# Optimization experiments

Hardware: AMD Instinct MI355X
Metric: run time of the kernel (lower is better)

## Reference

```python
import jax, jax.numpy as jnp
import numpy as np

T, B, N = 2048, 32, 1024   # time, batch, dan_hidden_size
H = 8                      # multihead_size
N2 = 128                   # attention_hidden_size
K = N // H                 # N_H = 128 per-head dim
K2 = N2 // H               # N2_H = 16 per-head attention dim


def setup_inputs() -> dict:
    key = jax.random.key(0)
    ks = jax.random.split(key, 10)
    s_n = 1.0 / np.sqrt(N)
    s_k = 1.0 / np.sqrt(K)
    s_k2 = 1.0 / np.sqrt(K2)
    return {
        "hyp": jax.random.normal(ks[0], (T, B, N), dtype=jnp.float32),
        # H independent per-head linears N -> K, stacked: (H, K, N)
        "Wmh": jax.random.uniform(ks[1], (H, K, N), minval=-s_n, maxval=s_n, dtype=jnp.float32),
        "bmh": jax.random.uniform(ks[2], (H, K), minval=-s_n, maxval=s_n, dtype=jnp.float32),
        # shared W: K -> K2
        "W": jax.random.uniform(ks[3], (K2, K), minval=-s_k, maxval=s_k, dtype=jnp.float32),
        "bW": jax.random.uniform(ks[4], (K2,), minval=-s_k, maxval=s_k, dtype=jnp.float32),
        # shared W_m: K -> K2
        "Wm": jax.random.uniform(ks[5], (K2, K), minval=-s_k, maxval=s_k, dtype=jnp.float32),
        "bWm": jax.random.uniform(ks[6], (K2,), minval=-s_k, maxval=s_k, dtype=jnp.float32),
        # shared W_h: K2 -> 1
        "Wh": jax.random.uniform(ks[7], (K2,), minval=-s_k2, maxval=s_k2, dtype=jnp.float32),
        "bWh": jax.random.uniform(ks[8], (), minval=-s_k2, maxval=s_k2, dtype=jnp.float32),
        "dan_hidden_size": N,
        "attention_hidden_size": N2,
        "multihead_size": H,
    }


def reference(hyp, Wmh, bmh, W, bW, Wm, bWm, Wh, bWh,
              dan_hidden_size, attention_hidden_size, multihead_size):
    # Per-head projections, all heads at once: (B, T, H, K)
    X = jnp.einsum('tbn,hkn->bthk', hyp, Wmh) + bmh
    # mean over time (original x.mean(0)): (B, H, K)
    m = X.mean(axis=1)
    # tanh-gated additive scoring: (B, T, H, K2)
    g = jnp.tanh(jnp.einsum('bthk,qk->bthq', X, W) + bW) \
        * jnp.tanh(jnp.einsum('bhk,qk->bhq', m, Wm) + bWm)[:, None]
    # scalar score per (b, t, h), softmax over time
    s = jnp.einsum('bthq,q->bth', g, Wh) + bWh
    a = jax.nn.softmax(s, axis=1)                       # (B, T, H)
    # attention-weighted sum over time: (B, H, K)
    c = jnp.einsum('bth,bthk->bhk', a, X)
    # concat heads along feature dim (head-major order, matches torch.cat)
    Bsz = c.shape[0]
    return c.reshape(Bsz, -1)                            # (B, N)
```

## Files before the change

### kernel.cpp

```cpp
#include <hip/hip_runtime.h>
#include <hip/hip_bf16.h>

#define T_DIM 2048
#define B_DIM 32
#define N_DIM 1024
#define H_DIM 8
#define K_DIM 128
#define Q_DIM 16

typedef __bf16 bf16x8 __attribute__((ext_vector_type(8)));
typedef __bf16 bf16x4 __attribute__((ext_vector_type(4)));
typedef float  f32x4  __attribute__((ext_vector_type(4)));

__device__ inline bf16x8 cvt8(float4 a, float4 b) {
    bf16x8 r;
    r[0] = (__bf16)a.x; r[1] = (__bf16)a.y; r[2] = (__bf16)a.z; r[3] = (__bf16)a.w;
    r[4] = (__bf16)b.x; r[5] = (__bf16)b.y; r[6] = (__bf16)b.z; r[7] = (__bf16)b.w;
    return r;
}

__global__ __launch_bounds__(256)
void cvt_f32_bf16(const float* __restrict__ s, __bf16* __restrict__ d)
{
    const long i = ((long)blockIdx.x * 256 + threadIdx.x) * 8;
    float4 a = *(const float4*)(s + i);
    float4 b = *(const float4*)(s + i + 4);
    *(bf16x8*)(d + i) = cvt8(a, b);
}

__global__ __launch_bounds__(512, 1)
void gemm_x_8ph(const __bf16* __restrict__ A, const __bf16* __restrict__ Bw,
                const float* __restrict__ bias, __bf16* __restrict__ X,
                float* __restrict__ mpart)
{
    __shared__ __bf16 ldsA[2][16384];
    __shared__ __bf16 ldsB[2][16384];
    __bf16* ldsAf = &ldsA[0][0];
    __bf16* ldsBf = &ldsB[0][0];

    const int tid  = threadIdx.x;
    const int lane = tid & 63;
    const int w    = tid >> 6;
    const int wm   = w >> 2;
    const int wn   = w & 3;

    const int bid  = blockIdx.x;
    const int wgid = (bid & 7) * 128 + (bid >> 3);
    const int bm   = wgid >> 2;
    const int bn   = wgid & 3;
    const long row0 = (long)bm * 256;
    const long col0 = (long)bn * 256;

    const int srow = w * 8 + (lane >> 3);
    const int scol = ((lane & 7) ^ (lane >> 3)) * 8;
    const __bf16* Ag = A  + (row0 + srow) * 1024 + scol;
    const __bf16* Bg = Bw + (col0 + srow) * 1024 + scol;
    const int ldst = w * 512;

    const int fr = lane & 15;
    const int g2 = lane >> 4;
    const int x7 = lane & 7;

    const __bf16* aK0 = ldsAf + (wm * 128 + fr) * 64 + ((g2    ) ^ x7) * 8;
    const __bf16* aK1 = ldsAf + (wm * 128 + fr) * 64 + ((4 + g2) ^ x7) * 8;
    const __bf16* bK0 = ldsBf + (wn * 64  + fr) * 64 + ((g2    ) ^ x7) * 8;
    const __bf16* bK1 = ldsBf + (wn * 64  + fr) * 64 + ((4 + g2) ^ x7) * 8;

    f32x4 acc[8][4];
    #pragma unroll
    for (int i = 0; i < 8; ++i)
        #pragma unroll
        for (int j = 0; j < 4; ++j)
            acc[i][j] = f32x4{0.f, 0.f, 0.f, 0.f};

    #define GLDA(SRC_, DST_) __builtin_amdgcn_global_load_lds( \
        (const __attribute__((address_space(1))) void*)(SRC_), \
        (__attribute__((address_space(3))) void*)(DST_), 16, 0, 0)

    #pragma unroll
    for (int j = 0; j < 2; ++j) GLDA(Ag + (long)j * 65536,          ldsAf + j * 4096 + ldst);
    #pragma unroll
    for (int j = 0; j < 2; ++j) GLDA(Ag + 131072 + (long)j * 65536, ldsAf + 8192 + j * 4096 + ldst);
    #pragma unroll
    for (int j = 0; j < 2; ++j) GLDA(Bg + (long)j * 65536,          ldsBf + j * 4096 + ldst);
    #pragma unroll
    for (int j = 0; j < 2; ++j) GLDA(Bg + 131072 + (long)j * 65536, ldsBf + 8192 + j * 4096 + ldst);
    #pragma unroll
    for (int j = 0; j < 2; ++j) GLDA(Bg + 64 + (long)j * 65536,          ldsBf + 16384 + j * 4096 + ldst);
    #pragma unroll
    for (int j = 0; j < 2; ++j) GLDA(Bg + 64 + 131072 + (long)j * 65536, ldsBf + 16384 + 8192 + j * 4096 + ldst);
    asm volatile("s_waitcnt vmcnt(4)" ::: "memory");
    __builtin_amdgcn_sched_barrier(0);
    __builtin_amdgcn_s_barrier();

    const __bf16* AgN = Ag + 64;
    const __bf16* BgN = Bg + 128;

    #define MFMA16(AF_, BF_, OFF_)                                             \
        __builtin_amdgcn_s_setprio(1);                                         \
        _Pragma("unroll") for (int mi = 0; mi < 4; ++mi)                       \
            _Pragma("unroll") for (int ni = 0; ni < 4; ++ni)                   \
                acc[mi + (OFF_)][ni] = __builtin_amdgcn_mfma_f32_16x16x32_bf16(\
                    BF_[ni], AF_[mi], acc[mi + (OFF_)][ni], 0, 0, 0);          \
        __builtin_amdgcn_s_setprio(0);

    #define LGKM0()                                                            \
        asm volatile("s_waitcnt lgkmcnt(0)" ::: "memory");                     \
        __builtin_amdgcn_sched_barrier(0);

    #define KTBODY(SO_, SN_, KO_, STGA_, STGB_, VM_)                           \
    {                                                                          \
        bf16x8 a0[4], b0[4], a0h[4], b1[4], a1[4], a1h[4];                     \
        _Pragma("unroll") for (int mi = 0; mi < 4; ++mi)                       \
            a0[mi] = *(const bf16x8*)(aK0 + (SO_) + mi * 1024);                \
        _Pragma("unroll") for (int ni = 0; ni < 4; ++ni)                       \
            b0[ni] = *(const bf16x8*)(bK0 + (SO_) + ni * 1024);                \
        if (STGA_) {                                                           \
            _Pragma("unroll") for (int j = 0; j < 2; ++j)                      \
                GLDA(AgN + (KO_) + (long)j * 65536,                            \
                     ldsAf + (SN_) + j * 4096 + ldst);                         \
        }                                                                      \
        __builtin_amdgcn_s_barrier();                                          \
        LGKM0();                                                               \
        MFMA16(a0, b0, 0);                                                     \
        __builtin_amdgcn_s_barrier();                                          \
        _Pragma("unroll") for (int mi = 0; mi < 4; ++mi)                       \
            a0h[mi] = *(const bf16x8*)(aK1 + (SO_) + mi * 1024);               \
        _Pragma("unroll") for (int ni = 0; ni < 4; ++ni)                       \
            b1[ni]  = *(const bf16x8*)(bK1 + (SO_) + ni * 1024);               \
        if (STGA_) {                                                           \
            _Pragma("unroll") for (int j = 0; j < 2; ++j)                      \
                GLDA(AgN + (KO_) + 131072 + (long)j * 65536,                   \
                     ldsAf + (SN_) + 8192 + j * 4096 + ldst);                  \
        }                                                                      \
        __builtin_amdgcn_s_barrier();                                          \
        LGKM0();                                                               \
        MFMA16(a0h, b1, 0);                                                    \
        __builtin_amdgcn_s_barrier();                                          \
        _Pragma("unroll") for (int mi = 0; mi < 4; ++mi)                       \
            a1[mi] = *(const bf16x8*)(aK0 + (SO_) + (mi + 4) * 1024);          \
        if (STGB_) {                                                           \
            _Pragma("unroll") for (int j = 0; j < 2; ++j)                      \
                GLDA(BgN + (KO_) + (long)j * 65536,                            \
                     ldsBf + (SO_) + j * 4096 + ldst);                         \
        }                                                                      \
        __builtin_amdgcn_s_barrier();                                          \
        LGKM0();                                                               \
        MFMA16(a1, b0, 4);                                                     \
        __builtin_amdgcn_s_barrier();                                          \
        _Pragma("unroll") for (int mi = 0; mi < 4; ++mi)                       \
            a1h[mi] = *(const bf16x8*)(aK1 + (SO_) + (mi + 4) * 1024);         \
        if (STGB_) {                                                           \
            _Pragma("unroll") for (int j = 0; j < 2; ++j)                      \
                GLDA(BgN + (KO_) + 131072 + (long)j * 65536,                   \
                     ldsBf + (SO_) + 8192 + j * 4096 + ldst);                  \
        }                                                                      \
        if ((VM_) == 4)      { asm volatile("s_waitcnt vmcnt(4)" ::: "memory"); } \
        else if ((VM_) == 0) { asm volatile("s_waitcnt vmcnt(0)" ::: "memory"); } \
        __builtin_amdgcn_sched_barrier(0);                                     \
        __builtin_amdgcn_s_barrier();                                          \
        LGKM0();                                                               \
        MFMA16(a1h, b1, 4);                                                    \
        __builtin_amdgcn_s_barrier();                                          \
    }

    #pragma unroll 1
    for (int ii = 0; ii < 7; ++ii) {
        KTBODY(0,     16384, 0,  1, 1, 4);
        KTBODY(16384, 0,     64, 1, 1, 4);
        AgN += 128; BgN += 128;
    }
    KTBODY(0,     16384, 0, 1, 0, 0);
    KTBODY(16384, 0,     0, 0, 0, -1);
    #undef KTBODY
    #undef MFMA16
    #undef LGKM0
    #undef GLDA

    const int g4 = lane >> 4;
    const long colb = col0 + wn * 64 + g4 * 4;

    float4 bias4[4];
    #pragma unroll
    for (int ni = 0; ni < 4; ++ni)
        bias4[ni] = *(const float4*)(bias + colb + ni * 16);

    f32x4 msum[2][4];
    #pragma unroll
    for (int bh = 0; bh < 2; ++bh)
        #pragma unroll
        for (int ni = 0; ni < 4; ++ni)
            msum[bh][ni] = f32x4{0.f, 0.f, 0.f, 0.f};

    #pragma unroll
    for (int mi = 0; mi < 8; ++mi) {
        const long row = row0 + wm * 128 + mi * 16 + fr;
        #pragma unroll
        for (int ni = 0; ni < 4; ++ni) {
            f32x4 xv;
            xv[0] = acc[mi][ni][0] + bias4[ni].x;
            xv[1] = acc[mi][ni][1] + bias4[ni].y;
            xv[2] = acc[mi][ni][2] + bias4[ni].z;
            xv[3] = acc[mi][ni][3] + bias4[ni].w;
            bf16x4 xb;
            xb[0] = (__bf16)xv[0]; xb[1] = (__bf16)xv[1];
            xb[2] = (__bf16)xv[2]; xb[3] = (__bf16)xv[3];
            *(bf16x4*)(X + row * 1024 + colb + ni * 16) = xb;
            msum[mi & 1][ni] += xv;
        }
    }

    float* ldsf = (float*)ldsAf;
    __syncthreads();
    if (wm == 1) {
        #pragma unroll
        for (int bh = 0; bh < 2; ++bh)
            #pragma unroll
            for (int ni = 0; ni < 4; ++ni)
                *(f32x4*)(ldsf + (bh * 16 + fr) * 256 + wn * 64 + ni * 16 + g4 * 4) = msum[bh][ni];
    }
    __syncthreads();
    if (wm == 0) {
        #pragma unroll
        for (int bh = 0; bh < 2; ++bh) {
            const int b = bh * 16 + fr;
            #pragma unroll
            for (int ni = 0; ni < 4; ++ni) {
                f32x4 other = *(const f32x4*)(ldsf + b * 256 + wn * 64 + ni * 16 + g4 * 4);
                f32x4 tot = msum[bh][ni] + other;
                *(f32x4*)(mpart + ((long)bm * 32 + b) * 1024 + colb + ni * 16) = tot;
            }
        }
    }
}

__global__ __launch_bounds__(256)
void gate2_k(const float* __restrict__ mpart, const float* __restrict__ Wm,
             const float* __restrict__ bWm, float* __restrict__ g2)
{
    __shared__ float mrow[1024];
    const int b = blockIdx.x;
    const int j4 = threadIdx.x * 4;
    f32x4 s = f32x4{0.f, 0.f, 0.f, 0.f};
    for (int bm = 0; bm < 256; ++bm)
        s += *(const f32x4*)(mpart + ((long)bm * 32 + b) * 1024 + j4);
    mrow[j4 + 0] = s[0] * (1.0f / 2048.0f);
    mrow[j4 + 1] = s[1] * (1.0f / 2048.0f);
    mrow[j4 + 2] = s[2] * (1.0f / 2048.0f);
    mrow[j4 + 3] = s[3] * (1.0f / 2048.0f);
    __syncthreads();
    if (threadIdx.x < 128) {
        const int h = threadIdx.x >> 4;
        const int q = threadIdx.x & 15;
        float d = bWm[q];
        #pragma unroll 8
        for (int k = 0; k < 128; ++k) d += mrow[h * 128 + k] * Wm[q * 128 + k];
        g2[(b * 8 + h) * 16 + q] = tanhf(d);
    }
}

__global__ __launch_bounds__(256)
void attn_part(const __bf16* __restrict__ X, const float* __restrict__ W,
               const float* __restrict__ bW, const float* __restrict__ g2,
               const float* __restrict__ Wh,
               float* __restrict__ partC, float* __restrict__ partML)
{
    __shared__ float sch[64];
    __shared__ float pl[64];
    __shared__ float red[1024];
    __shared__ float scal[3];

    const int tid  = threadIdx.x;
    const int lane = tid & 63;
    const int w    = tid >> 6;
    const int bx   = blockIdx.x;
    const int bh   = bx & 255;
    const int tc   = bx >> 8;
    const int b    = bh >> 3;
    const int h    = bh & 7;
    const int q    = lane & 15;
    const int g4   = lane >> 4;

    if (tid == 0) { scal[0] = -1e30f; scal[1] = 0.f; scal[2] = 0.f; }

    bf16x8 bfr[4];
    #pragma unroll
    for (int c = 0; c < 4; ++c) {
        const float* wp = W + q * 128 + c * 32 + g4 * 8;
        float4 w0 = *(const float4*)wp;
        float4 w1 = *(const float4*)(wp + 4);
        bfr[c] = cvt8(w0, w1);
    }
    const float whq = Wh[q];
    const float bWv = bW[q];
    const float gq  = g2[(b * 8 + h) * 16 + q];

    const long t0 = (long)tc * 256;
    const __bf16* xp = X + ((t0 + w * 16 + q) * 32 + b) * 1024 + h * 128 + g4 * 8;
    const int tr = tid >> 5;
    const int kq = tid & 31;
    const __bf16* xa = X + ((t0 + tr) * 32 + b) * 1024 + h * 128 + kq * 4;

    float c0 = 0.f, c1 = 0.f, c2 = 0.f, c3 = 0.f;

    __syncthreads();

    #pragma unroll 1
    for (int ch = 0; ch < 4; ++ch) {
        bf16x8 afr[4];
        #pragma unroll
        for (int c = 0; c < 4; ++c) afr[c] = *(const bf16x8*)(xp + c * 32);
        f32x4 acc = f32x4{0.f, 0.f, 0.f, 0.f};
        #pragma unroll
        for (int c = 0; c < 4; ++c)
            acc = __builtin_amdgcn_mfma_f32_16x16x32_bf16(afr[c], bfr[c], acc, 0, 0, 0);
        #pragma unroll
        for (int r = 0; r < 4; ++r) {
            float val = tanhf(acc[r] + bWv) * gq * whq;
            val += __shfl_xor(val, 1);
            val += __shfl_xor(val, 2);
            val += __shfl_xor(val, 4);
            val += __shfl_xor(val, 8);
            if (q == 0) sch[w * 16 + g4 * 4 + r] = val;
        }
        __syncthreads();

        if (tid < 64) {
            float v = sch[tid];
            float mx = v;
            #pragma unroll
            for (int off = 1; off < 64; off <<= 1)
                mx = fmaxf(mx, __shfl_xor(mx, off));
            const float mold = scal[0];
            const float newm = fmaxf(mold, mx);
            const float f    = __expf(mold - newm);
            const float p    = __expf(v - newm);
            pl[tid] = p;
            float ps = p;
            #pragma unroll
            for (int off = 1; off < 64; off <<= 1)
                ps += __shfl_xor(ps, off);
            if (tid == 0) {
                scal[0] = newm;
                scal[1] = f;
                scal[2] = scal[2] * f + ps;
            }
        }
        __syncthreads();

        const float f = scal[1];
        if (f != 1.0f) { c0 *= f; c1 *= f; c2 *= f; c3 *= f; }
        #pragma unroll
        for (int i = 0; i < 8; ++i) {
            const float p = pl[tr + 8 * i];
            bf16x4 xv = *(const bf16x4*)(xa + (long)(8 * i) * 32768);
            c0 += p * (float)xv[0];
            c1 += p * (float)xv[1];
            c2 += p * (float)xv[2];
            c3 += p * (float)xv[3];
        }
        __syncthreads();

        xp += 64 * 32768;
        xa += 64 * 32768;
    }

    red[tr * 128 + kq * 4 + 0] = c0;
    red[tr * 128 + kq * 4 + 1] = c1;
    red[tr * 128 + kq * 4 + 2] = c2;
    red[tr * 128 + kq * 4 + 3] = c3;
    __syncthreads();
    if (tid < 128) {
        float s = 0.f;
        #pragma unroll
        for (int r = 0; r < 8; ++r) s += red[r * 128 + tid];
        partC[((long)bh * 8 + tc) * 128 + tid] = s;
    }
    if (tid == 0) {
        partML[(bh * 8 + tc) * 2 + 0] = scal[0];
        partML[(bh * 8 + tc) * 2 + 1] = scal[2];
    }
}

__global__ __launch_bounds__(128)
void attn_merge(const float* __restrict__ partC, const float* __restrict__ partML,
                float* __restrict__ out)
{
    __shared__ float wgt[8];
    __shared__ float lsum;
    const int bh = blockIdx.x;
    const int k  = threadIdx.x;
    if (k == 0) {
        float m = -1e30f;
        #pragma unroll
        for (int tc = 0; tc < 8; ++tc) m = fmaxf(m, partML[(bh * 8 + tc) * 2]);
        float l = 0.f;
        #pragma unroll
        for (int tc = 0; tc < 8; ++tc) {
            float e = __expf(partML[(bh * 8 + tc) * 2] - m);
            wgt[tc] = e;
            l += partML[(bh * 8 + tc) * 2 + 1] * e;
        }
        lsum = l;
    }
    __syncthreads();
    float s = 0.f;
    #pragma unroll
    for (int tc = 0; tc < 8; ++tc)
        s += partC[((long)bh * 8 + tc) * 128 + k] * wgt[tc];
    const int b = bh >> 3;
    const int h = bh & 7;
    out[b * 1024 + h * 128 + k] = s / lsum;
}

extern "C" void kernel_launch(void* const* d_in, const int* in_sizes, int n_in,
                              void* d_out, int out_size, void* d_ws, size_t ws_size,
                              hipStream_t stream)
{
    const float* hyp = (const float*)d_in[0];
    const float* Wmh = (const float*)d_in[1];
    const float* bmh = (const float*)d_in[2];
    const float* W   = (const float*)d_in[3];
    const float* bW  = (const float*)d_in[4];
    const float* Wm  = (const float*)d_in[5];
    const float* bWm = (const float*)d_in[6];
    const float* Wh  = (const float*)d_in[7];
    float* out = (float*)d_out;

    char* ws = (char*)d_ws;
    const size_t SZ_X   = 134217728;
    const size_t SZ_AB  = 134217728;
    const size_t SZ_BB  = 2097152;
    const size_t SZ_MP  = 33554432;
    const size_t SZ_G2  = 16384;
    const size_t SZ_PC  = 1048576;
    const size_t SZ_PM  = 16384;

    size_t off = 0;
    __bf16* X      = (__bf16*)(ws + off); off += SZ_X;
    __bf16* Ab     = (__bf16*)(ws + off); off += SZ_AB;
    __bf16* Bb     = (__bf16*)(ws + off); off += SZ_BB;
    float*  mpart  = (float*) (ws + off); off += SZ_MP;
    float*  g2     = (float*) (ws + off); off += SZ_G2;
    float*  partC  = (float*) (ws + off); off += SZ_PC;
    float*  partML = (float*) (ws + off); off += SZ_PM;

    cvt_f32_bf16<<<32768, 256, 0, stream>>>(hyp, Ab);
    cvt_f32_bf16<<<512,   256, 0, stream>>>(Wmh, Bb);
    gemm_x_8ph<<<1024, 512, 0, stream>>>(Ab, Bb, bmh, X, mpart);
    gate2_k<<<32, 256, 0, stream>>>(mpart, Wm, bWm, g2);
    attn_part<<<2048, 256, 0, stream>>>(X, W, bW, g2, Wh, partC, partML);
    attn_merge<<<256, 128, 0, stream>>>(partC, partML, out);
}
```

Baseline: 298.8 us.

## Shrink GEMM tile to 128x256 with K=32 stages for multi-block occupancy

```diff
diff --git a/kernel.cpp b/kernel.cpp
--- a/kernel.cpp
+++ b/kernel.cpp
@@ -28,15 +28,14 @@
     *(bf16x8*)(d + i) = cvt8(a, b);
 }
 
-__global__ __launch_bounds__(512, 1)
+__global__ __launch_bounds__(512, 4)
 void gemm_x_8ph(const __bf16* __restrict__ A, const __bf16* __restrict__ Bw,
                 const float* __restrict__ bias, __bf16* __restrict__ X,
                 float* __restrict__ mpart)
 {
-    __shared__ __bf16 ldsA[2][16384];
-    __shared__ __bf16 ldsB[2][16384];
-    __bf16* ldsAf = &ldsA[0][0];
-    __bf16* ldsBf = &ldsB[0][0];
+    __shared__ char ldsraw[49152];
+    __bf16* ldsAf = (__bf16*)ldsraw;
+    __bf16* ldsBf = (__bf16*)(ldsraw + 16384);
 
     const int tid  = threadIdx.x;
     const int lane = tid & 63;
@@ -45,30 +44,26 @@
     const int wn   = w & 3;
 
     const int bid  = blockIdx.x;
-    const int wgid = (bid & 7) * 128 + (bid >> 3);
+    const int wgid = (bid & 7) * 256 + (bid >> 3);
     const int bm   = wgid >> 2;
     const int bn   = wgid & 3;
-    const long row0 = (long)bm * 256;
+    const long row0 = (long)bm * 128;
     const long col0 = (long)bn * 256;
 
-    const int srow = w * 8 + (lane >> 3);
-    const int scol = ((lane & 7) ^ (lane >> 3)) * 8;
+    const int srow = w * 16 + (lane >> 2);
+    const int scol = ((lane & 3) ^ ((lane >> 2) & 3)) * 8;
     const __bf16* Ag = A  + (row0 + srow) * 1024 + scol;
     const __bf16* Bg = Bw + (col0 + srow) * 1024 + scol;
     const int ldst = w * 512;
 
     const int fr = lane & 15;
     const int g2 = lane >> 4;
-    const int x7 = lane & 7;
-
-    const __bf16* aK0 = ldsAf + (wm * 128 + fr) * 64 + ((g2    ) ^ x7) * 8;
-    const __bf16* aK1 = ldsAf + (wm * 128 + fr) * 64 + ((4 + g2) ^ x7) * 8;
-    const __bf16* bK0 = ldsBf + (wn * 64  + fr) * 64 + ((g2    ) ^ x7) * 8;
-    const __bf16* bK1 = ldsBf + (wn * 64  + fr) * 64 + ((4 + g2) ^ x7) * 8;
-
-    f32x4 acc[8][4];
-    #pragma unroll
-    for (int i = 0; i < 8; ++i)
+    const __bf16* aK0 = ldsAf + (wm * 64 + fr) * 32 + ((g2 ^ (fr & 3)) * 8);
+    const __bf16* bK0 = ldsBf + (wn * 64 + fr) * 32 + ((g2 ^ (fr & 3)) * 8);
+
+    f32x4 acc[4][4];
+    #pragma unroll
+    for (int i = 0; i < 4; ++i)
         #pragma unroll
         for (int j = 0; j < 4; ++j)
             acc[i][j] = f32x4{0.f, 0.f, 0.f, 0.f};
@@ -77,103 +72,59 @@
         (const __attribute__((address_space(1))) void*)(SRC_), \
         (__attribute__((address_space(3))) void*)(DST_), 16, 0, 0)
 
-    #pragma unroll
-    for (int j = 0; j < 2; ++j) GLDA(Ag + (long)j * 65536,          ldsAf + j * 4096 + ldst);
-    #pragma unroll
-    for (int j = 0; j < 2; ++j) GLDA(Ag + 131072 + (long)j * 65536, ldsAf + 8192 + j * 4096 + ldst);
-    #pragma unroll
-    for (int j = 0; j < 2; ++j) GLDA(Bg + (long)j * 65536,          ldsBf + j * 4096 + ldst);
-    #pragma unroll
-    for (int j = 0; j < 2; ++j) GLDA(Bg + 131072 + (long)j * 65536, ldsBf + 8192 + j * 4096 + ldst);
-    #pragma unroll
-    for (int j = 0; j < 2; ++j) GLDA(Bg + 64 + (long)j * 65536,          ldsBf + 16384 + j * 4096 + ldst);
-    #pragma unroll
-    for (int j = 0; j < 2; ++j) GLDA(Bg + 64 + 131072 + (long)j * 65536, ldsBf + 16384 + 8192 + j * 4096 + ldst);
-    asm volatile("s_waitcnt vmcnt(4)" ::: "memory");
+    GLDA(Ag, ldsAf + ldst);
+    #pragma unroll
+    for (int j = 0; j < 2; ++j) GLDA(Bg + (long)j * 131072, ldsBf + j * 4096 + ldst);
+    GLDA(Ag + 32, ldsAf + 4096 + ldst);
+    #pragma unroll
+    for (int j = 0; j < 2; ++j) GLDA(Bg + 32 + (long)j * 131072, ldsBf + 8192 + j * 4096 + ldst);
+    asm volatile("s_waitcnt vmcnt(3)" ::: "memory");
     __builtin_amdgcn_sched_barrier(0);
     __builtin_amdgcn_s_barrier();
 
     const __bf16* AgN = Ag + 64;
-    const __bf16* BgN = Bg + 128;
-
-    #define MFMA16(AF_, BF_, OFF_)                                             \
+    const __bf16* BgN = Bg + 64;
+
+    #define LGKM0()                                                            \
+        asm volatile("s_waitcnt lgkmcnt(0)" ::: "memory");                     \
+        __builtin_amdgcn_sched_barrier(0);
+
+    #define KTBODY(SOA_, SOB_, KO_, STG_, VM_)                                 \
+    {                                                                          \
+        bf16x8 a0[4], b0[4];                                                   \
+        _Pragma("unroll") for (int mi = 0; mi < 4; ++mi)                       \
+            a0[mi] = *(const bf16x8*)(aK0 + (SOA_) + mi * 512);                \
+        _Pragma("unroll") for (int ni = 0; ni < 4; ++ni)                       \
+            b0[ni] = *(const bf16x8*)(bK0 + (SOB_) + ni * 512);                \
+        __builtin_amdgcn_s_barrier();                                          \
+        LGKM0();                                                               \
         __builtin_amdgcn_s_setprio(1);                                         \
         _Pragma("unroll") for (int mi = 0; mi < 4; ++mi)                       \
             _Pragma("unroll") for (int ni = 0; ni < 4; ++ni)                   \
-                acc[mi + (OFF_)][ni] = __builtin_amdgcn_mfma_f32_16x16x32_bf16(\
-                    BF_[ni], AF_[mi], acc[mi + (OFF_)][ni], 0, 0, 0);          \
-        __builtin_amdgcn_s_setprio(0);
-
-    #define LGKM0()                                                            \
-        asm volatile("s_waitcnt lgkmcnt(0)" ::: "memory");                     \
-        __builtin_amdgcn_sched_barrier(0);
-
-    #define KTBODY(SO_, SN_, KO_, STGA_, STGB_, VM_)                           \
-    {                                                                          \
-        bf16x8 a0[4], b0[4], a0h[4], b1[4], a1[4], a1h[4];                     \
-        _Pragma("unroll") for (int mi = 0; mi < 4; ++mi)                       \
-            a0[mi] = *(const bf16x8*)(aK0 + (SO_) + mi * 1024);                \
-        _Pragma("unroll") for (int ni = 0; ni < 4; ++ni)                       \
-            b0[ni] = *(const bf16x8*)(bK0 + (SO_) + ni * 1024);                \
-        if (STGA_) {                                                           \
+                acc[mi][ni] = __builtin_amdgcn_mfma_f32_16x16x32_bf16(         \
+                    b0[ni], a0[mi], acc[mi][ni], 0, 0, 0);                     \
+        __builtin_amdgcn_s_setprio(0);                                         \
+        if (STG_) {                                                            \
+            GLDA(AgN + (KO_), ldsAf + (SOA_) + ldst);                          \
             _Pragma("unroll") for (int j = 0; j < 2; ++j)                      \
-                GLDA(AgN + (KO_) + (long)j * 65536,                            \
-                     ldsAf + (SN_) + j * 4096 + ldst);                         \
+                GLDA(BgN + (KO_) + (long)j * 131072,                           \
+                     ldsBf + (SOB_) + j * 4096 + ldst);                        \
         }                                                                      \
-        __builtin_amdgcn_s_barrier();                                          \
-        LGKM0();                                                               \
-        MFMA16(a0, b0, 0);                                                     \
-        __builtin_amdgcn_s_barrier();                                          \
-        _Pragma("unroll") for (int mi = 0; mi < 4; ++mi)                       \
-            a0h[mi] = *(const bf16x8*)(aK1 + (SO_) + mi * 1024);               \
-        _Pragma("unroll") for (int ni = 0; ni < 4; ++ni)                       \
-            b1[ni]  = *(const bf16x8*)(bK1 + (SO_) + ni * 1024);               \
-        if (STGA_) {                                                           \
-            _Pragma("unroll") for (int j = 0; j < 2; ++j)                      \
-                GLDA(AgN + (KO_) + 131072 + (long)j * 65536,                   \
-                     ldsAf + (SN_) + 8192 + j * 4096 + ldst);                  \
-        }                                                                      \
-        __builtin_amdgcn_s_barrier();                                          \
-        LGKM0();                                                               \
-        MFMA16(a0h, b1, 0);                                                    \
-        __builtin_amdgcn_s_barrier();                                          \
-        _Pragma("unroll") for (int mi = 0; mi < 4; ++mi)                       \
-            a1[mi] = *(const bf16x8*)(aK0 + (SO_) + (mi + 4) * 1024);          \
-        if (STGB_) {                                                           \
-            _Pragma("unroll") for (int j = 0; j < 2; ++j)                      \
-                GLDA(BgN + (KO_) + (long)j * 65536,                            \
-                     ldsBf + (SO_) + j * 4096 + ldst);                         \
-        }                                                                      \
-        __builtin_amdgcn_s_barrier();                                          \
-        LGKM0();                                                               \
-        MFMA16(a1, b0, 4);                                                     \
-        __builtin_amdgcn_s_barrier();                                          \
-        _Pragma("unroll") for (int mi = 0; mi < 4; ++mi)                       \
-            a1h[mi] = *(const bf16x8*)(aK1 + (SO_) + (mi + 4) * 1024);         \
-        if (STGB_) {                                                           \
-            _Pragma("unroll") for (int j = 0; j < 2; ++j)                      \
-                GLDA(BgN + (KO_) + 131072 + (long)j * 65536,                   \
-                     ldsBf + (SO_) + 8192 + j * 4096 + ldst);                  \
-        }                                                                      \
-        if ((VM_) == 4)      { asm volatile("s_waitcnt vmcnt(4)" ::: "memory"); } \
+        if ((VM_) == 3)      { asm volatile("s_waitcnt vmcnt(3)" ::: "memory"); } \
         else if ((VM_) == 0) { asm volatile("s_waitcnt vmcnt(0)" ::: "memory"); } \
         __builtin_amdgcn_sched_barrier(0);                                     \
         __builtin_amdgcn_s_barrier();                                          \
-        LGKM0();                                                               \
-        MFMA16(a1h, b1, 4);                                                    \
-        __builtin_amdgcn_s_barrier();                                          \
     }
 
     #pragma unroll 1
-    for (int ii = 0; ii < 7; ++ii) {
-        KTBODY(0,     16384, 0,  1, 1, 4);
-        KTBODY(16384, 0,     64, 1, 1, 4);
-        AgN += 128; BgN += 128;
-    }
-    KTBODY(0,     16384, 0, 1, 0, 0);
-    KTBODY(16384, 0,     0, 0, 0, -1);
+    for (int ii = 0; ii < 15; ++ii) {
+        KTBODY(0,    0,    0,  1, 3);
+        KTBODY(4096, 8192, 32, 1, 3);
+        AgN += 64; BgN += 64;
+    }
+    KTBODY(0,    0,    0, 0, 0);
+    KTBODY(4096, 8192, 0, 0, -1);
     #undef KTBODY
-    #undef MFMA16
     #undef LGKM0
     #undef GLDA
 
@@ -193,8 +144,8 @@
             msum[bh][ni] = f32x4{0.f, 0.f, 0.f, 0.f};
 
     #pragma unroll
-    for (int mi = 0; mi < 8; ++mi) {
-        const long row = row0 + wm * 128 + mi * 16 + fr;
+    for (int mi = 0; mi < 4; ++mi) {
+        const long row = row0 + wm * 64 + mi * 16 + fr;
         #pragma unroll
         for (int ni = 0; ni < 4; ++ni) {
             f32x4 xv;
@@ -210,7 +161,7 @@
         }
     }
 
-    float* ldsf = (float*)ldsAf;
+    float* ldsf = (float*)ldsraw;
     __syncthreads();
     if (wm == 1) {
         #pragma unroll
@@ -242,7 +193,7 @@
     const int b = blockIdx.x;
     const int j4 = threadIdx.x * 4;
     f32x4 s = f32x4{0.f, 0.f, 0.f, 0.f};
-    for (int bm = 0; bm < 256; ++bm)
+    for (int bm = 0; bm < 512; ++bm)
         s += *(const f32x4*)(mpart + ((long)bm * 32 + b) * 1024 + j4);
     mrow[j4 + 0] = s[0] * (1.0f / 2048.0f);
     mrow[j4 + 1] = s[1] * (1.0f / 2048.0f);
@@ -431,7 +382,7 @@
     const size_t SZ_X   = 134217728;
     const size_t SZ_AB  = 134217728;
     const size_t SZ_BB  = 2097152;
-    const size_t SZ_MP  = 33554432;
+    const size_t SZ_MP  = 67108864;
     const size_t SZ_G2  = 16384;
     const size_t SZ_PC  = 1048576;
     const size_t SZ_PM  = 16384;
@@ -447,7 +398,7 @@
 
     cvt_f32_bf16<<<32768, 256, 0, stream>>>(hyp, Ab);
     cvt_f32_bf16<<<512,   256, 0, stream>>>(Wmh, Bb);
-    gemm_x_8ph<<<1024, 512, 0, stream>>>(Ab, Bb, bmh, X, mpart);
+    gemm_x_8ph<<<2048, 512, 0, stream>>>(Ab, Bb, bmh, X, mpart);
     gate2_k<<<32, 256, 0, stream>>>(mpart, Wm, bWm, g2);
     attn_part<<<2048, 256, 0, stream>>>(X, W, bW, g2, Wh, partC, partML);
     attn_merge<<<256, 128, 0, stream>>>(partC, partML, out);
```

Result: slower. 331.7 us, median of 4 (+11.0%).
